# Optimization experiments

Measured on AMD Instinct MI355X. Metric: run time of the kernel, lower is better.

## Reference

```python
import jax, jax.numpy as jnp
import numpy as np
from jax import lax

TEMPERATURES = (0.05, 0.1, 0.2)
MASK_SELF = True


def _cdist(a, b):
    # Euclidean distance matrix [Na, Nb], matches torch.cdist(p=2)
    d2 = (jnp.sum(a * a, axis=1)[:, None]
          + jnp.sum(b * b, axis=1)[None, :]
          - 2.0 * (a @ b.T))
    return jnp.sqrt(jnp.maximum(d2, 0.0))


def setup_inputs() -> dict:
    key = jax.random.key(0)
    k1, k2, k3 = jax.random.split(key, 3)
    N, N_pos, D = 4096, 4096, 256
    x = jax.random.normal(k1, (N, D), dtype=jnp.float32)
    y_pos = jax.random.normal(k2, (N_pos, D), dtype=jnp.float32)
    y_neg = jax.random.normal(k3, (N, D), dtype=jnp.float32)
    return {"x": x, "y_pos": y_pos, "y_neg": y_neg}


def reference(x, y_pos, y_neg):
    N, D = x.shape
    N_neg = y_neg.shape[0]

    dist_pos = _cdist(x, y_pos)            # [N, N_pos]
    dist_neg = _cdist(x, y_neg)            # [N, N_neg]
    if MASK_SELF:
        dist_neg = dist_neg + jnp.eye(N, dtype=x.dtype) * 1e6

    # temperature auto-scale, detached in original (torch.no_grad)
    mean_dist = lax.stop_gradient(jnp.mean(dist_pos))

    dist = jnp.concatenate([dist_neg, dist_pos], axis=1)  # [N, N_neg+N_pos]

    V_total = jnp.zeros_like(x)
    for T in TEMPERATURES:
        adaptive_T = T * mean_dist
        log_kernel = jnp.maximum(-dist / adaptive_T, -80.0)
        kernel = jnp.exp(log_kernel)
        row_sum = jnp.sum(kernel, axis=-1, keepdims=True)   # [N, 1]
        col_sum = jnp.sum(kernel, axis=-2, keepdims=True)   # [1, N_neg+N_pos]
        normalizer = jnp.sqrt(jnp.maximum(row_sum * col_sum, 1e-12))
        A = kernel / normalizer
        A_neg = A[:, :N_neg]
        A_pos = A[:, N_neg:]
        # second-order reweighting
        W_pos = A_pos * jnp.sum(A_neg, axis=-1, keepdims=True)
        W_neg = A_neg * jnp.sum(A_pos, axis=-1, keepdims=True)
        V_total = V_total + (W_pos @ y_pos - W_neg @ y_neg)

    target = lax.stop_gradient(x + V_total)
    loss = jnp.mean((x - target) ** 2)
    return loss
```

## Files before the change

kernel.cpp:

```cpp
#include <hip/hip_runtime.h>

#define NROWS 4096
#define DCOLS 8192
#define DIM   256
#define NHALF 4096

typedef __attribute__((ext_vector_type(8))) short bf16x8;
typedef __attribute__((ext_vector_type(4))) float f32x4;
typedef __attribute__((ext_vector_type(4))) unsigned short ushort4v;
typedef __attribute__((ext_vector_type(2))) _Float16 half2v;
typedef __attribute__((ext_vector_type(4))) _Float16 half4v;
typedef __attribute__((ext_vector_type(8))) _Float16 half8;

#define LN128 4.852030263919617f
#define MEAN_DIV (1.0 / 2097152.0)

static __device__ __forceinline__ unsigned short f2bf(float f) {
  union { float f; unsigned int i; } v; v.f = f;
  unsigned int x = v.i;
  return (unsigned short)((x + 0x7fffu + ((x >> 16) & 1u)) >> 16);
}

static __device__ __forceinline__ half2v cvt_pk(float a, float b) {
  return __builtin_bit_cast(half2v, __builtin_amdgcn_cvt_pkrtz(a, b));
}

static __device__ __forceinline__ half8 fp8x8_to_h8(int lo, int hi) {
  auto p0 = __builtin_amdgcn_cvt_pk_f32_fp8(lo, false);
  auto p1 = __builtin_amdgcn_cvt_pk_f32_fp8(lo, true);
  auto p2 = __builtin_amdgcn_cvt_pk_f32_fp8(hi, false);
  auto p3 = __builtin_amdgcn_cvt_pk_f32_fp8(hi, true);
  half2v h0 = cvt_pk(p0[0], p0[1]);
  half2v h1 = cvt_pk(p1[0], p1[1]);
  half2v h2 = cvt_pk(p2[0], p2[1]);
  half2v h3 = cvt_pk(p3[0], p3[1]);
  return (half8){h0[0], h0[1], h1[0], h1[1], h2[0], h2[1], h3[0], h3[1]};
}

static __device__ __forceinline__ void gload_lds16(const void* g, void* l) {
  __builtin_amdgcn_global_load_lds(
      (const __attribute__((address_space(1))) void*)g,
      (__attribute__((address_space(3))) void*)l, 16, 0, 0);
}

static __device__ __forceinline__ float hsum8(half8 v) {
  float s = 0.f;
  #pragma unroll
  for (int u = 0; u < 8; ++u) s += (float)v[u];
  return s;
}

#define WREDUCE(v) { v += __shfl_xor(v, 1); v += __shfl_xor(v, 2); v += __shfl_xor(v, 4); \
                     v += __shfl_xor(v, 8); v += __shfl_xor(v, 16); v += __shfl_xor(v, 32); }

__global__ __launch_bounds__(256) void k_prep(
    const float* __restrict__ x, const float* __restrict__ ypos,
    const float* __restrict__ yneg, unsigned short* __restrict__ xb,
    unsigned short* __restrict__ yb, float* __restrict__ xx, float* __restrict__ yy) {
  const int lane = threadIdx.x & 63, w = threadIdx.x >> 6;
  const int b = blockIdx.x * 4 + w;
  const float* src; unsigned short* dst; float* nrm;
  if (b < 4096)      { src = x + (size_t)b * DIM;             dst = xb + (size_t)b * DIM;            nrm = xx + b; }
  else if (b < 8192) { int r = b - 4096; src = yneg + (size_t)r * DIM; dst = yb + (size_t)r * DIM;   nrm = yy + r; }
  else               { int r = b - 8192; src = ypos + (size_t)r * DIM; dst = yb + (size_t)(NHALF + r) * DIM; nrm = yy + NHALF + r; }
  float4 v = *(const float4*)(src + lane * 4);
  ushort4v ov = { f2bf(v.x), f2bf(v.y), f2bf(v.z), f2bf(v.w) };
  *(ushort4v*)(dst + lane * 4) = ov;
  float s = v.x * v.x + v.y * v.y + v.z * v.z + v.w * v.w;
  WREDUCE(s);
  if (lane == 0) nrm[0] = s;
}

__global__ __launch_bounds__(256) void k_transpose(
    const float* __restrict__ ypos, const float* __restrict__ yneg,
    unsigned short* __restrict__ ybt) {
  __shared__ unsigned short tile[64][68];
  int r0 = blockIdx.x * 64;
  int c0 = blockIdx.y * 64;
  const float* src = (r0 < NHALF) ? (yneg + (size_t)r0 * DIM)
                                  : (ypos + (size_t)(r0 - NHALF) * DIM);
  int tx = threadIdx.x & 63, ty = threadIdx.x >> 6;
  #pragma unroll
  for (int it = 0; it < 16; ++it) {
    int r = it * 4 + ty;
    _Float16 h = (_Float16)src[(size_t)r * DIM + c0 + tx];
    tile[r][tx] = __builtin_bit_cast(unsigned short, h);
  }
  __syncthreads();
  #pragma unroll
  for (int it = 0; it < 16; ++it) {
    int c = it * 4 + ty;
    ybt[(size_t)(c0 + c) * DCOLS + r0 + tx] = tile[tx][c];
  }
}

__global__ __launch_bounds__(256) void k_mean(
    const unsigned short* __restrict__ xb, const unsigned short* __restrict__ yb,
    const float* __restrict__ xx, const float* __restrict__ yy,
    double* __restrict__ meanacc) {
  __shared__ unsigned short As[128 * 64];
  __shared__ unsigned short Bs[128 * 64];
  __shared__ float red[4];
  const int bj = NHALF + blockIdx.x * 128;
  const int bi = blockIdx.y * 128;
  const int tid = threadIdx.x;
  const int lane = tid & 63, wid = tid >> 6;
  const int wr = wid >> 1, wc = wid & 1;
  f32x4 acc[4][4];
  #pragma unroll
  for (int m = 0; m < 4; ++m)
    #pragma unroll
    for (int n = 0; n < 4; ++n) acc[m][n] = (f32x4){0.f, 0.f, 0.f, 0.f};

  for (int k0 = 0; k0 < DIM; k0 += 64) {
    __syncthreads();
    #pragma unroll
    for (int it = 0; it < 4; ++it) {
      int L = it * 256 + tid;
      int row = L >> 3;
      int cb = (L & 7) * 16;
      int cbs = cb ^ ((row & 7) << 4);
      gload_lds16(xb + (size_t)(bi + row) * DIM + k0 + (cbs >> 1), (char*)As + L * 16);
      gload_lds16(yb + (size_t)(bj + row) * DIM + k0 + (cbs >> 1), (char*)Bs + L * 16);
    }
    __syncthreads();
    #pragma unroll
    for (int kk = 0; kk < 2; ++kk) {
      bf16x8 a[4], b[4];
      #pragma unroll
      for (int m = 0; m < 4; ++m) {
        int row = wr * 64 + m * 16 + (lane & 15);
        int cb = (kk * 64 + ((lane >> 4) * 16)) ^ ((row & 7) << 4);
        a[m] = *(const bf16x8*)((const char*)As + row * 128 + cb);
      }
      #pragma unroll
      for (int n = 0; n < 4; ++n) {
        int row = wc * 64 + n * 16 + (lane & 15);
        int cb = (kk * 64 + ((lane >> 4) * 16)) ^ ((row & 7) << 4);
        b[n] = *(const bf16x8*)((const char*)Bs + row * 128 + cb);
      }
      #pragma unroll
      for (int m = 0; m < 4; ++m)
        #pragma unroll
        for (int n = 0; n < 4; ++n)
          acc[m][n] = __builtin_amdgcn_mfma_f32_16x16x32_bf16(a[m], b[n], acc[m][n], 0, 0, 0);
    }
  }

  float xv[16], yv[4];
  #pragma unroll
  for (int m = 0; m < 4; ++m)
    #pragma unroll
    for (int r = 0; r < 4; ++r)
      xv[m * 4 + r] = xx[bi + wr * 64 + m * 16 + (lane >> 4) * 4 + r];
  #pragma unroll
  for (int n = 0; n < 4; ++n)
    yv[n] = yy[bj + wc * 64 + n * 16 + (lane & 15)];

  float lsum = 0.f;
  #pragma unroll
  for (int m = 0; m < 4; ++m)
    #pragma unroll
    for (int n = 0; n < 4; ++n)
      #pragma unroll
      for (int r = 0; r < 4; ++r) {
        float d2 = xv[m * 4 + r] + yv[n] - 2.f * acc[m][n][r];
        lsum += sqrtf(fmaxf(d2, 0.f));
      }
  WREDUCE(lsum);
  if (lane == 0) red[wid] = lsum;
  __syncthreads();
  if (tid == 0) atomicAdd(meanacc, (double)(red[0] + red[1] + red[2] + red[3]));
}

__global__ __launch_bounds__(256) void k_diste(
    const unsigned short* __restrict__ xb, const unsigned short* __restrict__ yb,
    const float* __restrict__ xx, const float* __restrict__ yy,
    const double* __restrict__ meanacc, unsigned char* __restrict__ ebuf,
    float* __restrict__ cs_part) {
  __shared__ __align__(16) char lds[32768];
  unsigned short* As = (unsigned short*)lds;
  unsigned short* Bs = (unsigned short*)(lds + 16384);
  const int bid = blockIdx.x;
  const int xcd = bid & 7, lcl = bid >> 3;
  const int jb = xcd * 8 + (lcl & 7), ib = lcl >> 3;
  const int bj = jb * 128;
  const int bi = ib * 128;
  const int tid = threadIdx.x;
  const int lane = tid & 63, wid = tid >> 6;
  const int wr = wid >> 1, wc = wid & 1;
  f32x4 acc[4][4];
  #pragma unroll
  for (int m = 0; m < 4; ++m)
    #pragma unroll
    for (int n = 0; n < 4; ++n) acc[m][n] = (f32x4){0.f, 0.f, 0.f, 0.f};

  for (int k0 = 0; k0 < DIM; k0 += 64) {
    __syncthreads();
    #pragma unroll
    for (int it = 0; it < 4; ++it) {
      int L = it * 256 + tid;
      int cb = (L & 7) * 16;
      int row = L >> 3;
      int cbs = cb ^ ((row & 7) << 4);
      gload_lds16(xb + (size_t)(bi + row) * DIM + k0 + (cbs >> 1), (char*)As + L * 16);
      gload_lds16(yb + (size_t)(bj + row) * DIM + k0 + (cbs >> 1), (char*)Bs + L * 16);
    }
    __syncthreads();
    #pragma unroll
    for (int kk = 0; kk < 2; ++kk) {
      bf16x8 a[4], b[4];
      #pragma unroll
      for (int m = 0; m < 4; ++m) {
        int row = wr * 64 + m * 16 + (lane & 15);
        int cb = (kk * 64 + ((lane >> 4) * 16)) ^ ((row & 7) << 4);
        a[m] = *(const bf16x8*)((const char*)As + row * 128 + cb);
      }
      #pragma unroll
      for (int n = 0; n < 4; ++n) {
        int row = wc * 64 + n * 16 + (lane & 15);
        int cb = (kk * 64 + ((lane >> 4) * 16)) ^ ((row & 7) << 4);
        b[n] = *(const bf16x8*)((const char*)Bs + row * 128 + cb);
      }
      #pragma unroll
      for (int m = 0; m < 4; ++m)
        #pragma unroll
        for (int n = 0; n < 4; ++n)
          acc[m][n] = __builtin_amdgcn_mfma_f32_16x16x32_bf16(a[m], b[n], acc[m][n], 0, 0, 0);
    }
  }

  const float md = (float)(meanacc[0] * MEAN_DIV);
  const float ia2 = 1.f / (0.2f * md);
  float xv[16], yv[4];
  #pragma unroll
  for (int m = 0; m < 4; ++m)
    #pragma unroll
    for (int r = 0; r < 4; ++r)
      xv[m * 4 + r] = xx[bi + wr * 64 + m * 16 + (lane >> 4) * 4 + r];
  #pragma unroll
  for (int n = 0; n < 4; ++n)
    yv[n] = yy[bj + wc * 64 + n * 16 + (lane & 15)];

  const bool hasdiag = (bi == bj);
  __syncthreads();

  half2v cq4[4] = {}, cq2[4] = {}, cq1[4] = {};
  #pragma unroll
  for (int m = 0; m < 4; ++m) {
    const int r0 = wr * 64 + m * 16 + (lane >> 4) * 4;
    #pragma unroll
    for (int n = 0; n < 4; ++n) {
      const int col = wc * 64 + n * 16 + (lane & 15);
      float q[4];
      #pragma unroll
      for (int r = 0; r < 4; ++r) {
        float d2 = xv[m * 4 + r] + yv[n] - 2.f * acc[m][n][r];
        float d = sqrtf(fmaxf(d2, 0.f));
        q[r] = __expf(fmaf(d, -ia2, LN128));
      }
      if (hasdiag) {
        #pragma unroll
        for (int r = 0; r < 4; ++r)
          if (r0 + r == col) q[r] = 0.f;
      }
      half2v p01 = cvt_pk(q[0], q[1]);
      half2v p23 = cvt_pk(q[2], q[3]);
      half2v q2a = p01 * p01, q2b = p23 * p23;
      half2v q4a = q2a * q2a, q4b = q2b * q2b;
      cq1[n] += p01; cq1[n] += p23;
      cq2[n] += q2a; cq2[n] += q2b;
      cq4[n] += q4a; cq4[n] += q4b;
      *(_Float16*)(lds + (r0 + 0) * 256 + ((col * 2) ^ (((r0 + 0) & 7) << 4))) = p01[0];
      *(_Float16*)(lds + (r0 + 1) * 256 + ((col * 2) ^ (((r0 + 1) & 7) << 4))) = p01[1];
      *(_Float16*)(lds + (r0 + 2) * 256 + ((col * 2) ^ (((r0 + 2) & 7) << 4))) = p23[0];
      *(_Float16*)(lds + (r0 + 3) * 256 + ((col * 2) ^ (((r0 + 3) & 7) << 4))) = p23[1];
    }
  }
  float csf[3][4];
  #pragma unroll
  for (int n = 0; n < 4; ++n) {
    csf[0][n] = (float)cq4[n][0] + (float)cq4[n][1];
    csf[1][n] = (float)cq2[n][0] + (float)cq2[n][1];
    csf[2][n] = (float)cq1[n][0] + (float)cq1[n][1];
  }
  #pragma unroll
  for (int p = 0; p < 3; ++p)
    #pragma unroll
    for (int n = 0; n < 4; ++n) {
      float v = csf[p][n];
      v += __shfl_xor(v, 16); v += __shfl_xor(v, 32);
      csf[p][n] = v;
    }
  if (lane < 16) {
    const int slab = ib * 2 + wr;
    #pragma unroll
    for (int p = 0; p < 3; ++p)
      #pragma unroll
      for (int n = 0; n < 4; ++n)
        cs_part[(size_t)slab * 24576 + p * 8192 + bj + wc * 64 + n * 16 + lane] = csf[p][n];
  }
  __syncthreads();
  #pragma unroll
  for (int it = 0; it < 8; ++it) {
    int chunk = it * 256 + tid;
    int row = chunk >> 4;
    int cb16 = (chunk & 15) * 16;
    half8 h = *(const half8*)(lds + row * 256 + (cb16 ^ ((row & 7) << 4)));
    int w0 = __builtin_amdgcn_cvt_pk_fp8_f32((float)h[0], (float)h[1], 0, false);
    w0 = __builtin_amdgcn_cvt_pk_fp8_f32((float)h[2], (float)h[3], w0, true);
    int w1 = __builtin_amdgcn_cvt_pk_fp8_f32((float)h[4], (float)h[5], 0, false);
    w1 = __builtin_amdgcn_cvt_pk_fp8_f32((float)h[6], (float)h[7], w1, true);
    int2 outv = { w0, w1 };
    *(int2*)(ebuf + (size_t)(bi + row) * DCOLS + bj + (chunk & 15) * 8) = outv;
  }
}

__global__ __launch_bounds__(256) void k_csred(
    const float* __restrict__ cs_part, _Float16* __restrict__ ich) {
  int idx = blockIdx.x * 256 + threadIdx.x;
  float s = 0.f;
  #pragma unroll 8
  for (int sl = 0; sl < 64; ++sl) s += cs_part[(size_t)sl * 24576 + idx];
  ich[idx] = (_Float16)rsqrtf(s);
}

__global__ __launch_bounds__(256) void k_rowstat(
    const unsigned char* __restrict__ ebuf, const _Float16* __restrict__ ich,
    float* __restrict__ gtab) {
  __shared__ float red[4][9];
  const int i = blockIdx.x;
  const int t = threadIdx.x;
  const int lane = t & 63, w = t >> 6;
  const unsigned char* erow = ebuf + (size_t)i * DCOLS;
  half8 r4a = {}, r2a = {}, r1a = {};
  half8 sn4 = {}, sn2 = {}, sn1 = {}, sp4 = {}, sp2 = {}, sp1 = {};
  #pragma unroll
  for (int it = 0; it < 4; ++it) {
    int j0 = it * 2048 + t * 8;
    int2 wd = *(const int2*)(erow + j0);
    half8 e = fp8x8_to_h8(wd.x, wd.y);
    half8 e2 = e * e, e4 = e2 * e2;
    half8 c0 = *(const half8*)(ich + j0);
    half8 c1 = *(const half8*)(ich + 8192 + j0);
    half8 c2 = *(const half8*)(ich + 16384 + j0);
    r4a += e4; r2a += e2; r1a += e;
    if (it < 2) { sn4 += e4 * c0; sn2 += e2 * c1; sn1 += e * c2; }
    else        { sp4 += e4 * c0; sp2 += e2 * c1; sp1 += e * c2; }
  }
  float v0 = hsum8(r4a), v1 = hsum8(r2a), v2 = hsum8(r1a);
  float v3 = hsum8(sn4), v4 = hsum8(sn2), v5 = hsum8(sn1);
  float v6 = hsum8(sp4), v7 = hsum8(sp2), v8 = hsum8(sp1);
  WREDUCE(v0); WREDUCE(v1); WREDUCE(v2);
  WREDUCE(v3); WREDUCE(v4); WREDUCE(v5);
  WREDUCE(v6); WREDUCE(v7); WREDUCE(v8);
  if (lane == 0) {
    red[w][0] = v0; red[w][1] = v1; red[w][2] = v2;
    red[w][3] = v3; red[w][4] = v4; red[w][5] = v5;
    red[w][6] = v6; red[w][7] = v7; red[w][8] = v8;
  }
  __syncthreads();
  if (t < 9) red[0][t] = red[0][t] + red[1][t] + red[2][t] + red[3][t];
  __syncthreads();
  if (t < 3) {
    float R = red[0][t], Sn = red[0][3 + t], Sp = red[0][6 + t];
    gtab[i * 8 + t] = -Sp / R;
    gtab[i * 8 + 4 + t] = Sn / R;
  }
}

__global__ __launch_bounds__(512) void k_flash(
    const unsigned char* __restrict__ ebuf, const unsigned short* __restrict__ ybt,
    const _Float16* __restrict__ ich, const float* __restrict__ gtab,
    _Float16* __restrict__ vpart) {
  __shared__ __align__(16) char lds[81920];
  const int jc = blockIdx.x;
  const int rb = blockIdx.y;
  const int j0base = jc * 1024;
  const int tid = threadIdx.x;
  const int lane = tid & 63, wid = tid >> 6;
  const int wr = wid >> 2, wc = wid & 3;
  const int crow = tid >> 3;
  const int cjA = (tid & 7) * 16;
  const float* gp = gtab + (size_t)(rb * 64 + crow) * 8 + (jc < 4 ? 0 : 4);
  const _Float16 g0h = (_Float16)gp[0], g1h = (_Float16)gp[1], g2h = (_Float16)gp[2];
  const half8 g0v = {g0h, g0h, g0h, g0h, g0h, g0h, g0h, g0h};
  const half8 g1v = {g1h, g1h, g1h, g1h, g1h, g1h, g1h, g1h};
  const half8 g2v = {g2h, g2h, g2h, g2h, g2h, g2h, g2h, g2h};
  const unsigned char* erowp = ebuf + (size_t)(rb * 64 + crow) * DCOLS;

  f32x4 acc[2][4];
  #pragma unroll
  for (int m = 0; m < 2; ++m)
    #pragma unroll
    for (int n = 0; n < 4; ++n) acc[m][n] = (f32x4){0.f, 0.f, 0.f, 0.f};

  for (int jt = 0; jt < 8; ++jt) {
    const int j0 = j0base + jt * 128;
    __syncthreads();
    #pragma unroll
    for (int it = 0; it < 8; ++it) {
      int L = it * 512 + tid;
      int row = L >> 4;
      int cb = (L & 15) * 16;
      int cbs = cb ^ ((row & 7) << 4);
      gload_lds16(ybt + (size_t)row * DCOLS + j0 + (cbs >> 1), lds + 16384 + L * 16);
    }
    {
      int4 wd = *(const int4*)(erowp + j0 + cjA);
      half8 ea = fp8x8_to_h8(wd.x, wd.y);
      half8 eb = fp8x8_to_h8(wd.z, wd.w);
      #pragma unroll
      for (int u2 = 0; u2 < 2; ++u2) {
        half8 e = u2 ? eb : ea;
        half8 e2 = e * e, e4 = e2 * e2;
        const int joff = cjA + u2 * 8;
        half8 c0 = *(const half8*)(ich + j0 + joff);
        half8 c1 = *(const half8*)(ich + 8192 + j0 + joff);
        half8 c2 = *(const half8*)(ich + 16384 + j0 + joff);
        half8 C8 = (e4 * c0) * g0v + (e2 * c1) * g1v + (e * c2) * g2v;
        *(half8*)(lds + crow * 256 + ((joff * 2) ^ ((crow & 7) << 4))) = C8;
      }
    }
    __syncthreads();
    #pragma unroll
    for (int kk = 0; kk < 4; ++kk) {
      half8 a[2], b[4];
      #pragma unroll
      for (int m = 0; m < 2; ++m) {
        int row = wr * 32 + m * 16 + (lane & 15);
        int cb = (kk * 64 + ((lane >> 4) * 16)) ^ ((row & 7) << 4);
        a[m] = *(const half8*)(lds + row * 256 + cb);
      }
      #pragma unroll
      for (int n = 0; n < 4; ++n) {
        int row = wc * 64 + n * 16 + (lane & 15);
        int cb = (kk * 64 + ((lane >> 4) * 16)) ^ ((row & 7) << 4);
        b[n] = *(const half8*)(lds + 16384 + row * 256 + cb);
      }
      #pragma unroll
      for (int m = 0; m < 2; ++m)
        #pragma unroll
        for (int n = 0; n < 4; ++n)
          acc[m][n] = __builtin_amdgcn_mfma_f32_16x16x32_f16(a[m], b[n], acc[m][n], 0, 0, 0);
    }
  }
  #pragma unroll
  for (int m = 0; m < 2; ++m)
    #pragma unroll
    for (int n = 0; n < 4; ++n)
      #pragma unroll
      for (int r = 0; r < 4; ++r) {
        int gi = rb * 64 + wr * 32 + m * 16 + (lane >> 4) * 4 + r;
        int gd = wc * 64 + n * 16 + (lane & 15);
        vpart[(size_t)jc * 1048576 + (size_t)gi * 256 + gd] = (_Float16)acc[m][n][r];
      }
}

__global__ __launch_bounds__(256) void k_loss(
    const _Float16* __restrict__ vpart, float* __restrict__ ploss) {
  const int tid = blockIdx.x * 256 + threadIdx.x;
  const size_t e0 = (size_t)tid * 8;
  float vv[8] = {0, 0, 0, 0, 0, 0, 0, 0};
  #pragma unroll
  for (int sl = 0; sl < 8; ++sl) {
    half8 h = *(const half8*)(vpart + (size_t)sl * 1048576 + e0);
    #pragma unroll
    for (int u = 0; u < 8; ++u) vv[u] += (float)h[u];
  }
  float s = 0.f;
  #pragma unroll
  for (int u = 0; u < 8; ++u) s += vv[u] * vv[u];
  WREDUCE(s);
  __shared__ float red[4];
  if ((threadIdx.x & 63) == 0) red[threadIdx.x >> 6] = s;
  __syncthreads();
  if (threadIdx.x == 0) ploss[blockIdx.x] = red[0] + red[1] + red[2] + red[3];
}

__global__ __launch_bounds__(256) void k_finish(
    const float* __restrict__ ploss, float* __restrict__ out) {
  float v = ploss[threadIdx.x] + ploss[threadIdx.x + 256];
  WREDUCE(v);
  __shared__ float red[4];
  if ((threadIdx.x & 63) == 0) red[threadIdx.x >> 6] = v;
  __syncthreads();
  if (threadIdx.x == 0)
    out[0] = (float)((double)(red[0] + red[1] + red[2] + red[3]) / 1048576.0);
}

extern "C" void kernel_launch(void* const* d_in, const int* in_sizes, int n_in,
                              void* d_out, int out_size, void* d_ws, size_t ws_size,
                              hipStream_t stream) {
  (void)in_sizes; (void)n_in; (void)out_size; (void)ws_size;
  const float* x    = (const float*)d_in[0];
  const float* ypos = (const float*)d_in[1];
  const float* yneg = (const float*)d_in[2];

  char* ws = (char*)d_ws;
  size_t o = 0;
  unsigned char* dist = (unsigned char*)(ws + o); o += (size_t)NROWS * DCOLS;
  unsigned short* xb   = (unsigned short*)(ws + o); o += (size_t)NROWS * DIM * 2;
  unsigned short* yb   = (unsigned short*)(ws + o); o += (size_t)DCOLS * DIM * 2;
  unsigned short* ybt  = (unsigned short*)(ws + o); o += (size_t)DCOLS * DIM * 2;
  float* xx      = (float*)(ws + o); o += NROWS * 4;
  float* yy      = (float*)(ws + o); o += DCOLS * 4;
  double* meanacc = (double*)(ws + o); o += 256;
  _Float16* ich  = (_Float16*)(ws + o); o += 3 * DCOLS * 2;
  float* gtab    = (float*)(ws + o); o += (size_t)NROWS * 8 * 4;
  float* ploss   = (float*)(ws + o); o += 512 * 4;
  float* cs_part = (float*)(ws + o);
  _Float16* vpart = (_Float16*)(ws + o); o += (size_t)8 * NROWS * DIM * 2;

  hipMemsetAsync(meanacc, 0, 8, stream);
  k_prep<<<3072, 256, 0, stream>>>(x, ypos, yneg, xb, yb, xx, yy);
  k_transpose<<<dim3(128, 4), 256, 0, stream>>>(ypos, yneg, ybt);
  k_mean<<<dim3(32, 4), 256, 0, stream>>>(xb, yb, xx, yy, meanacc);
  k_diste<<<2048, 256, 0, stream>>>(xb, yb, xx, yy, meanacc, dist, cs_part);
  k_csred<<<96, 256, 0, stream>>>(cs_part, ich);
  k_rowstat<<<4096, 256, 0, stream>>>(dist, ich, gtab);
  k_flash<<<dim3(8, 64), 512, 0, stream>>>(dist, ybt, ich, gtab, vpart);
  k_loss<<<512, 256, 0, stream>>>(vpart, ploss);
  k_finish<<<1, 256, 0, stream>>>(ploss, (float*)d_out);
}
```

Before: 130.5 us.

## Double-buffer LDS tiles in distance and flash kernels to overlap loads with MFMA

After: 138.2 us. 1.06x slower.

```diff
diff --git a/kernel.cpp b/kernel.cpp
--- a/kernel.cpp
+++ b/kernel.cpp
@@ -178,9 +178,7 @@
     const float* __restrict__ xx, const float* __restrict__ yy,
     const double* __restrict__ meanacc, unsigned char* __restrict__ ebuf,
     float* __restrict__ cs_part) {
-  __shared__ __align__(16) char lds[32768];
-  unsigned short* As = (unsigned short*)lds;
-  unsigned short* Bs = (unsigned short*)(lds + 16384);
+  __shared__ __align__(16) char lds[65536];
   const int bid = blockIdx.x;
   const int xcd = bid & 7, lcl = bid >> 3;
   const int jb = xcd * 8 + (lcl & 7), ib = lcl >> 3;
@@ -195,18 +193,32 @@
     #pragma unroll
     for (int n = 0; n < 4; ++n) acc[m][n] = (f32x4){0.f, 0.f, 0.f, 0.f};
 
-  for (int k0 = 0; k0 < DIM; k0 += 64) {
-    __syncthreads();
-    #pragma unroll
-    for (int it = 0; it < 4; ++it) {
-      int L = it * 256 + tid;
-      int cb = (L & 7) * 16;
-      int row = L >> 3;
-      int cbs = cb ^ ((row & 7) << 4);
-      gload_lds16(xb + (size_t)(bi + row) * DIM + k0 + (cbs >> 1), (char*)As + L * 16);
-      gload_lds16(yb + (size_t)(bj + row) * DIM + k0 + (cbs >> 1), (char*)Bs + L * 16);
-    }
-    __syncthreads();
+  #pragma unroll
+  for (int it = 0; it < 4; ++it) {
+    int L = it * 256 + tid;
+    int cb = (L & 7) * 16;
+    int row = L >> 3;
+    int cbs = cb ^ ((row & 7) << 4);
+    gload_lds16(xb + (size_t)(bi + row) * DIM + (cbs >> 1), lds + L * 16);
+    gload_lds16(yb + (size_t)(bj + row) * DIM + (cbs >> 1), lds + 16384 + L * 16);
+  }
+  __syncthreads();
+
+  for (int k = 0; k < 4; ++k) {
+    const int cur = (k & 1) << 15;
+    if (k < 3) {
+      const int nxt = ((k + 1) & 1) << 15;
+      const int k0 = (k + 1) * 64;
+      #pragma unroll
+      for (int it = 0; it < 4; ++it) {
+        int L = it * 256 + tid;
+        int cb = (L & 7) * 16;
+        int row = L >> 3;
+        int cbs = cb ^ ((row & 7) << 4);
+        gload_lds16(xb + (size_t)(bi + row) * DIM + k0 + (cbs >> 1), lds + nxt + L * 16);
+        gload_lds16(yb + (size_t)(bj + row) * DIM + k0 + (cbs >> 1), lds + nxt + 16384 + L * 16);
+      }
+    }
     #pragma unroll
     for (int kk = 0; kk < 2; ++kk) {
       bf16x8 a[4], b[4];
@@ -214,13 +226,13 @@
       for (int m = 0; m < 4; ++m) {
         int row = wr * 64 + m * 16 + (lane & 15);
         int cb = (kk * 64 + ((lane >> 4) * 16)) ^ ((row & 7) << 4);
-        a[m] = *(const bf16x8*)((const char*)As + row * 128 + cb);
+        a[m] = *(const bf16x8*)(lds + cur + row * 128 + cb);
       }
       #pragma unroll
       for (int n = 0; n < 4; ++n) {
         int row = wc * 64 + n * 16 + (lane & 15);
         int cb = (kk * 64 + ((lane >> 4) * 16)) ^ ((row & 7) << 4);
-        b[n] = *(const bf16x8*)((const char*)Bs + row * 128 + cb);
+        b[n] = *(const bf16x8*)(lds + cur + 16384 + row * 128 + cb);
       }
       #pragma unroll
       for (int m = 0; m < 4; ++m)
@@ -228,6 +240,7 @@
         for (int n = 0; n < 4; ++n)
           acc[m][n] = __builtin_amdgcn_mfma_f32_16x16x32_bf16(a[m], b[n], acc[m][n], 0, 0, 0);
     }
+    __syncthreads();
   }
 
   const float md = (float)(meanacc[0] * MEAN_DIV);
@@ -243,7 +256,6 @@
     yv[n] = yy[bj + wc * 64 + n * 16 + (lane & 15)];
 
   const bool hasdiag = (bi == bj);
-  __syncthreads();
 
   half2v cq4[4] = {}, cq2[4] = {}, cq1[4] = {};
   #pragma unroll
@@ -381,13 +393,14 @@
   const int lane = tid & 63, wid = tid >> 6;
   const int wr = wid >> 2, wc = wid & 3;
   const int crow = tid >> 3;
-  const int cjA = (tid & 7) * 16;
+  const int cj8 = (tid & 7) * 8;
   const float* gp = gtab + (size_t)(rb * 64 + crow) * 8 + (jc < 4 ? 0 : 4);
   const _Float16 g0h = (_Float16)gp[0], g1h = (_Float16)gp[1], g2h = (_Float16)gp[2];
   const half8 g0v = {g0h, g0h, g0h, g0h, g0h, g0h, g0h, g0h};
   const half8 g1v = {g1h, g1h, g1h, g1h, g1h, g1h, g1h, g1h};
   const half8 g2v = {g2h, g2h, g2h, g2h, g2h, g2h, g2h, g2h};
   const unsigned char* erowp = ebuf + (size_t)(rb * 64 + crow) * DCOLS;
+  const int ctwb = crow * 128 + ((cj8 * 2) ^ ((crow & 7) << 4));
 
   f32x4 acc[2][4];
   #pragma unroll
@@ -395,48 +408,62 @@
     #pragma unroll
     for (int n = 0; n < 4; ++n) acc[m][n] = (f32x4){0.f, 0.f, 0.f, 0.f};
 
-  for (int jt = 0; jt < 8; ++jt) {
-    const int j0 = j0base + jt * 128;
-    __syncthreads();
-    #pragma unroll
-    for (int it = 0; it < 8; ++it) {
-      int L = it * 512 + tid;
-      int row = L >> 4;
-      int cb = (L & 15) * 16;
-      int cbs = cb ^ ((row & 7) << 4);
-      gload_lds16(ybt + (size_t)row * DCOLS + j0 + (cbs >> 1), lds + 16384 + L * 16);
-    }
-    {
-      int4 wd = *(const int4*)(erowp + j0 + cjA);
-      half8 ea = fp8x8_to_h8(wd.x, wd.y);
-      half8 eb = fp8x8_to_h8(wd.z, wd.w);
-      #pragma unroll
-      for (int u2 = 0; u2 < 2; ++u2) {
-        half8 e = u2 ? eb : ea;
-        half8 e2 = e * e, e4 = e2 * e2;
-        const int joff = cjA + u2 * 8;
-        half8 c0 = *(const half8*)(ich + j0 + joff);
-        half8 c1 = *(const half8*)(ich + 8192 + j0 + joff);
-        half8 c2 = *(const half8*)(ich + 16384 + j0 + joff);
-        half8 C8 = (e4 * c0) * g0v + (e2 * c1) * g1v + (e * c2) * g2v;
-        *(half8*)(lds + crow * 256 + ((joff * 2) ^ ((crow & 7) << 4))) = C8;
-      }
-    }
-    __syncthreads();
-    #pragma unroll
-    for (int kk = 0; kk < 4; ++kk) {
+  #pragma unroll
+  for (int it = 0; it < 4; ++it) {
+    int L = it * 512 + tid;
+    int row = L >> 3;
+    int cb = (L & 7) * 16;
+    int cbs = cb ^ ((row & 7) << 4);
+    gload_lds16(ybt + (size_t)row * DCOLS + j0base + (cbs >> 1), lds + 16384 + L * 16);
+  }
+  {
+    int2 wd = *(const int2*)(erowp + j0base + cj8);
+    half8 c0 = *(const half8*)(ich + j0base + cj8);
+    half8 c1 = *(const half8*)(ich + 8192 + j0base + cj8);
+    half8 c2 = *(const half8*)(ich + 16384 + j0base + cj8);
+    half8 e = fp8x8_to_h8(wd.x, wd.y);
+    half8 e2 = e * e, e4 = e2 * e2;
+    half8 C8 = (e4 * c0) * g0v + (e2 * c1) * g1v + (e * c2) * g2v;
+    *(half8*)(lds + ctwb) = C8;
+  }
+  __syncthreads();
+
+  #pragma unroll 2
+  for (int jt = 0; jt < 16; ++jt) {
+    const int cur = jt & 1;
+    const int ctc = cur * 8192;
+    const int bsc = 16384 + cur * 32768;
+    int2 wd; half8 c0, c1, c2;
+    if (jt < 15) {
+      const int j1 = j0base + (jt + 1) * 64;
+      const int bsn = 16384 + (cur ^ 1) * 32768;
+      #pragma unroll
+      for (int it = 0; it < 4; ++it) {
+        int L = it * 512 + tid;
+        int row = L >> 3;
+        int cb = (L & 7) * 16;
+        int cbs = cb ^ ((row & 7) << 4);
+        gload_lds16(ybt + (size_t)row * DCOLS + j1 + (cbs >> 1), lds + bsn + L * 16);
+      }
+      wd = *(const int2*)(erowp + j1 + cj8);
+      c0 = *(const half8*)(ich + j1 + cj8);
+      c1 = *(const half8*)(ich + 8192 + j1 + cj8);
+      c2 = *(const half8*)(ich + 16384 + j1 + cj8);
+    }
+    #pragma unroll
+    for (int kk = 0; kk < 2; ++kk) {
       half8 a[2], b[4];
       #pragma unroll
       for (int m = 0; m < 2; ++m) {
         int row = wr * 32 + m * 16 + (lane & 15);
         int cb = (kk * 64 + ((lane >> 4) * 16)) ^ ((row & 7) << 4);
-        a[m] = *(const half8*)(lds + row * 256 + cb);
+        a[m] = *(const half8*)(lds + ctc + row * 128 + cb);
       }
       #pragma unroll
       for (int n = 0; n < 4; ++n) {
         int row = wc * 64 + n * 16 + (lane & 15);
         int cb = (kk * 64 + ((lane >> 4) * 16)) ^ ((row & 7) << 4);
-        b[n] = *(const half8*)(lds + 16384 + row * 256 + cb);
+        b[n] = *(const half8*)(lds + bsc + row * 128 + cb);
       }
       #pragma unroll
       for (int m = 0; m < 2; ++m)
@@ -444,6 +471,13 @@
         for (int n = 0; n < 4; ++n)
           acc[m][n] = __builtin_amdgcn_mfma_f32_16x16x32_f16(a[m], b[n], acc[m][n], 0, 0, 0);
     }
+    if (jt < 15) {
+      half8 e = fp8x8_to_h8(wd.x, wd.y);
+      half8 e2 = e * e, e4 = e2 * e2;
+      half8 C8 = (e4 * c0) * g0v + (e2 * c1) * g1v + (e * c2) * g2v;
+      *(half8*)(lds + (cur ^ 1) * 8192 + ctwb) = C8;
+    }
+    __syncthreads();
   }
   #pragma unroll
   for (int m = 0; m < 2; ++m)
```
